# Kernel tuning notes

Measured on AMD Instinct MI355X. Metric: run time of the kernel, lower is better.

## Reference

```python
import jax, jax.numpy as jnp
import numpy as np

NEG_INF = float(np.finfo(np.float32).min)
CHUNK = 8
EPS = 1e-6
NOISE_STD = 1.0
SHARP = 1.0


def exclusive_cumsum(x):
    # [a,b,c] -> [0,a,a+b]
    return jnp.cumsum(jnp.pad(x[:, :-1], ((0, 0), (1, 0))), axis=1)


def moving_sum(x, back, forward):
    # x: [B, K]; out[i] = sum x[i-back : i+forward+1], via cumsum difference
    w = back + forward + 1
    xp = jnp.pad(x, ((0, 0), (back, forward)))
    cs = jnp.pad(jnp.cumsum(xp, axis=1), ((0, 0), (1, 0)))
    return cs[:, w:] - cs[:, :-w]


def setup_inputs() -> dict:
    key = jax.random.key(0)
    ks = jax.random.split(key, 12)
    B, K, D, A = 64, 2000, 512, 512
    s = 0.02
    inp = {
        'key': jax.random.normal(ks[0], (B, K, D), jnp.float32),
        'value': jax.random.normal(ks[1], (B, K, D), jnp.float32),
        'query': jax.random.normal(ks[2], (B, 1, D), jnp.float32),
        'mask': jnp.ones((B, 1, K), jnp.int32),
        'aw_prev': jnp.zeros((B, K), jnp.float32).at[:, 0].set(1.0),
        'noise': jax.random.normal(ks[3], (B, K), jnp.float32),
        'Wk_mono': jax.random.normal(ks[4], (D, A), jnp.float32) * s,
        'bk_mono': jnp.zeros((A,), jnp.float32),
        'Wq_mono': jax.random.normal(ks[5], (D, A), jnp.float32) * s,
        'bq_mono': jnp.zeros((A,), jnp.float32),
        'r': jnp.full((1,), -4.0, jnp.float32),
        'Wk_chunk': jax.random.normal(ks[6], (D, A), jnp.float32) * s,
        'bk_chunk': jnp.zeros((A,), jnp.float32),
        'Wq_chunk': jax.random.normal(ks[7], (D, A), jnp.float32) * s,
        'bq_chunk': jnp.zeros((A,), jnp.float32),
    }
    return inp


def reference(key, value, query, mask, aw_prev, noise,
              Wk_mono, bk_mono, Wq_mono, bq_mono, r,
              Wk_chunk, bk_chunk, Wq_chunk, bq_chunk):
    B, K, _ = key.shape
    adim = Wk_mono.shape[1]
    scale = jnp.sqrt(jnp.asarray(adim, jnp.float32))
    m = mask.reshape(B, K) != 0  # qlen == 1

    # ---- monotonic energy (scaled_dot) ----
    k_m = key @ Wk_mono + bk_mono              # [B,K,A]
    q_m = query @ Wq_mono + bq_mono            # [B,1,A]
    e_mono = jnp.einsum('bqa,bka->bk', q_m, k_m) / scale + r[0]
    e_mono = jnp.where(m, e_mono, NEG_INF)

    # ---- parallel-mode monotonic alignment ----
    p = jax.nn.sigmoid(e_mono + noise * NOISE_STD)             # p_choose_i
    cumprod_1mp = jnp.exp(exclusive_cumsum(jnp.log(jnp.clip(1.0 - p, EPS, 1.0))))
    alpha = p * cumprod_1mp * jnp.cumsum(
        aw_prev / jnp.clip(cumprod_1mp, EPS, 1.0), axis=1)     # [B,K]

    # ---- chunkwise attention ----
    k_c = key @ Wk_chunk + bk_chunk
    q_c = query @ Wq_chunk + bq_chunk
    e_c = jnp.einsum('bqa,bka->bk', q_c, k_c) / scale
    e_c = jnp.where(m, e_c, NEG_INF)
    e_c = e_c - jnp.max(e_c, axis=1, keepdims=True)
    sm_exp = jnp.clip(jnp.exp(e_c), 1e-5, None)
    denom = moving_sum(sm_exp, CHUNK - 1, 0)
    beta = sm_exp * moving_sum(alpha * SHARP / denom, 0, CHUNK - 1)  # [B,K]

    # ---- context vector ----
    cv = jnp.einsum('bk,bkd->bd', beta, value)[:, None, :]     # [B,1,D]
    return cv, alpha
```

## Files before the change

### kernel.cpp

```cpp
#include <hip/hip_runtime.h>
#include <hip/hip_bf16.h>

#define B_N    64
#define K_LEN  2000
#define D_DIM  512
#define NEG_INF (-3.402823466e38f)
#define EPS_C  1e-6f
#define INV_SCALE (1.0f/22.62741699796952f)

__global__ __launch_bounds__(256) void proj_kernel(
    const float* __restrict__ query,
    const float* __restrict__ Wq_m, const float* __restrict__ bq_m,
    const float* __restrict__ Wq_c, const float* __restrict__ bq_c,
    const float* __restrict__ Wk_m, const float* __restrict__ bk_m,
    const float* __restrict__ Wk_c, const float* __restrict__ bk_c,
    const float* __restrict__ r,
    float* __restrict__ v_all, float* __restrict__ c_all)
{
    const int b = blockIdx.x, br = blockIdx.y, t = threadIdx.x;
    const float* Wq = br ? Wq_c : Wq_m;
    const float* bq = br ? bq_c : bq_m;
    const float* Wk = br ? Wk_c : Wk_m;
    const float* bk = br ? bk_c : bk_m;
    __shared__ float qs[D_DIM];
    __shared__ float qv[D_DIM];
    __shared__ float red[256];
    for (int i = t; i < D_DIM; i += 256) qs[i] = query[(size_t)b*D_DIM + i];
    __syncthreads();
    for (int a = t; a < D_DIM; a += 256) {
        float a0 = 0.f, a1 = 0.f, a2 = 0.f, a3 = 0.f;
        #pragma unroll 4
        for (int d = 0; d < D_DIM; d += 4) {
            a0 = fmaf(qs[d+0], Wq[(size_t)(d+0)*D_DIM + a], a0);
            a1 = fmaf(qs[d+1], Wq[(size_t)(d+1)*D_DIM + a], a1);
            a2 = fmaf(qs[d+2], Wq[(size_t)(d+2)*D_DIM + a], a2);
            a3 = fmaf(qs[d+3], Wq[(size_t)(d+3)*D_DIM + a], a3);
        }
        qv[a] = (a0 + a1) + (a2 + a3) + bq[a];
    }
    __syncthreads();
    for (int d = t; d < D_DIM; d += 256) {
        const float4* row = (const float4*)(Wk + (size_t)d*D_DIM);
        const float4* q4 = (const float4*)qv;
        float acc = 0.f;
        #pragma unroll 4
        for (int a4 = 0; a4 < D_DIM/4; ++a4) {
            float4 w = row[a4], q = q4[a4];
            acc = fmaf(w.x, q.x, acc); acc = fmaf(w.y, q.y, acc);
            acc = fmaf(w.z, q.z, acc); acc = fmaf(w.w, q.w, acc);
        }
        v_all[((size_t)b*2 + br)*D_DIM + d] = acc * INV_SCALE;
    }
    float part = 0.f;
    for (int a = t; a < D_DIM; a += 256) part = fmaf(qv[a], bk[a], part);
    red[t] = part; __syncthreads();
    for (int s = 128; s; s >>= 1) { if (t < s) red[t] += red[t + s]; __syncthreads(); }
    if (t == 0) c_all[b*2 + br] = red[0] * INV_SCALE + (br ? 0.f : r[0]);
}

__global__ __launch_bounds__(256) void energy_kernel(
    const float* __restrict__ key, const int* __restrict__ mask,
    const float* __restrict__ v_all, const float* __restrict__ c_all,
    float* __restrict__ e_mono, float* __restrict__ e_c)
{
    const int b = blockIdx.x;
    const int kb0 = blockIdx.y * 125;
    const int kend = kb0 + 125;
    const int lane = threadIdx.x & 63;
    const int wave = threadIdx.x >> 6;
    const float4* vm4 = (const float4*)(v_all + ((size_t)b*2 + 0)*D_DIM);
    const float4* vc4 = (const float4*)(v_all + ((size_t)b*2 + 1)*D_DIM);
    const float4 vmA = vm4[lane*2], vmB = vm4[lane*2 + 1];
    const float4 vcA = vc4[lane*2], vcB = vc4[lane*2 + 1];
    const float cm = c_all[b*2 + 0], cc = c_all[b*2 + 1];

    for (int k = kb0 + wave; k < kend; k += 8) {
        const int k2 = k + 4;
        const bool has2 = (k2 < kend);
        const float4* kr0 = (const float4*)(key + ((size_t)b*K_LEN + k)*D_DIM);
        const float4* kr1 = (const float4*)(key + ((size_t)b*K_LEN + (has2 ? k2 : k))*D_DIM);
        float4 a0 = kr0[lane*2], b0 = kr0[lane*2 + 1];
        float4 a1 = kr1[lane*2], b1 = kr1[lane*2 + 1];
        float dm0 = 0.f, dc0 = 0.f, dm1 = 0.f, dc1 = 0.f;
        dm0 = fmaf(a0.x, vmA.x, dm0); dm0 = fmaf(a0.y, vmA.y, dm0);
        dm0 = fmaf(a0.z, vmA.z, dm0); dm0 = fmaf(a0.w, vmA.w, dm0);
        dm0 = fmaf(b0.x, vmB.x, dm0); dm0 = fmaf(b0.y, vmB.y, dm0);
        dm0 = fmaf(b0.z, vmB.z, dm0); dm0 = fmaf(b0.w, vmB.w, dm0);
        dc0 = fmaf(a0.x, vcA.x, dc0); dc0 = fmaf(a0.y, vcA.y, dc0);
        dc0 = fmaf(a0.z, vcA.z, dc0); dc0 = fmaf(a0.w, vcA.w, dc0);
        dc0 = fmaf(b0.x, vcB.x, dc0); dc0 = fmaf(b0.y, vcB.y, dc0);
        dc0 = fmaf(b0.z, vcB.z, dc0); dc0 = fmaf(b0.w, vcB.w, dc0);
        dm1 = fmaf(a1.x, vmA.x, dm1); dm1 = fmaf(a1.y, vmA.y, dm1);
        dm1 = fmaf(a1.z, vmA.z, dm1); dm1 = fmaf(a1.w, vmA.w, dm1);
        dm1 = fmaf(b1.x, vmB.x, dm1); dm1 = fmaf(b1.y, vmB.y, dm1);
        dm1 = fmaf(b1.z, vmB.z, dm1); dm1 = fmaf(b1.w, vmB.w, dm1);
        dc1 = fmaf(a1.x, vcA.x, dc1); dc1 = fmaf(a1.y, vcA.y, dc1);
        dc1 = fmaf(a1.z, vcA.z, dc1); dc1 = fmaf(a1.w, vcA.w, dc1);
        dc1 = fmaf(b1.x, vcB.x, dc1); dc1 = fmaf(b1.y, vcB.y, dc1);
        dc1 = fmaf(b1.z, vcB.z, dc1); dc1 = fmaf(b1.w, vcB.w, dc1);
        #pragma unroll
        for (int off = 32; off; off >>= 1) {
            dm0 += __shfl_xor(dm0, off); dc0 += __shfl_xor(dc0, off);
            dm1 += __shfl_xor(dm1, off); dc1 += __shfl_xor(dc1, off);
        }
        if (lane == 0) {
            size_t gk = (size_t)b*K_LEN + k;
            bool mk = mask[gk] != 0;
            e_mono[gk] = mk ? dm0 + cm : NEG_INF;
            e_c[gk]    = mk ? dc0 + cc : NEG_INF;
            if (has2) {
                size_t gk2 = (size_t)b*K_LEN + k2;
                bool mk2 = mask[gk2] != 0;
                e_mono[gk2] = mk2 ? dm1 + cm : NEG_INF;
                e_c[gk2]    = mk2 ? dc1 + cc : NEG_INF;
            }
        }
    }
}

__global__ __launch_bounds__(256) void scan_kernel(
    const float* __restrict__ e_mono_g, const float* __restrict__ e_c_g,
    const float* __restrict__ noise, const float* __restrict__ aw_prev,
    float* __restrict__ alpha_out, float* __restrict__ beta_out)
{
    const int b = blockIdx.x, t = threadIdx.x;
    const int lane = t & 63, wv = t >> 6;
    __shared__ float sal[2048];
    __shared__ float sse[2048];
    __shared__ float su[2048];
    __shared__ float wsA[4], wsB[4], wsM[4];

    const float* em = e_mono_g + (size_t)b*K_LEN;
    const float* ec = e_c_g   + (size_t)b*K_LEN;
    const float* nz = noise   + (size_t)b*K_LEN;
    const float* aw = aw_prev + (size_t)b*K_LEN;

    const int base = t*8;
    float p[8], lg[8];
    #pragma unroll
    for (int j = 0; j < 8; ++j) {
        const int k = base + j;
        float pv = 0.f, lv = 0.f, ecv = NEG_INF;
        if (k < K_LEN) {
            float e = em[k] + nz[k];
            pv = 1.f / (1.f + __expf(-e) * 1.0f);
            pv = 1.f / (1.f + expf(-e));
            float om = fminf(fmaxf(1.f - pv, EPS_C), 1.f);
            lv = logf(om);
            ecv = ec[k];
        }
        p[j] = pv; lg[j] = lv; sse[k] = ecv;
    }

    float ex[8]; float run = 0.f;
    #pragma unroll
    for (int j = 0; j < 8; ++j) { ex[j] = run; run += lg[j]; }
    float incl = run;
    #pragma unroll
    for (int off = 1; off < 64; off <<= 1) {
        float v = __shfl_up(incl, off, 64);
        if (lane >= off) incl += v;
    }
    if (lane == 63) wsA[wv] = incl;
    __syncthreads();
    float wpre = 0.f;
    #pragma unroll
    for (int w = 0; w < 4; ++w) if (w < wv) wpre += wsA[w];
    const float pre = wpre + incl - run;

    float cp[8], t2i[8]; float run2 = 0.f;
    #pragma unroll
    for (int j = 0; j < 8; ++j) {
        const int k = base + j;
        float c = expf(pre + ex[j]);
        cp[j] = c;
        float t2 = 0.f;
        if (k < K_LEN) t2 = aw[k] / fminf(fmaxf(c, EPS_C), 1.f);
        run2 += t2; t2i[j] = run2;
    }
    float incl2 = run2;
    #pragma unroll
    for (int off = 1; off < 64; off <<= 1) {
        float v = __shfl_up(incl2, off, 64);
        if (lane >= off) incl2 += v;
    }
    if (lane == 63) wsB[wv] = incl2;
    __syncthreads();
    float wpre2 = 0.f;
    #pragma unroll
    for (int w = 0; w < 4; ++w) if (w < wv) wpre2 += wsB[w];
    const float pre2 = wpre2 + incl2 - run2;
    #pragma unroll
    for (int j = 0; j < 8; ++j) {
        const int k = base + j;
        float al = p[j] * cp[j] * (pre2 + t2i[j]);
        sal[k] = al;
        if (k < K_LEN) alpha_out[(size_t)b*K_LEN + k] = al;
    }
    __syncthreads();

    float mx = NEG_INF;
    for (int k = t; k < 2048; k += 256) mx = fmaxf(mx, sse[k]);
    #pragma unroll
    for (int off = 32; off; off >>= 1) mx = fmaxf(mx, __shfl_xor(mx, off));
    if (lane == 0) wsM[wv] = mx;
    __syncthreads();
    mx = fmaxf(fmaxf(wsM[0], wsM[1]), fmaxf(wsM[2], wsM[3]));

    for (int k = t; k < 2048; k += 256) {
        float se = 0.f;
        if (k < K_LEN) se = fmaxf(expf(sse[k] - mx), 1e-5f);
        sse[k] = se;
    }
    __syncthreads();
    for (int k = t; k < 2048; k += 256) {
        float u = 0.f;
        if (k < K_LEN) {
            float den = 0.f;
            int j0 = (k > 7) ? (k - 7) : 0;
            for (int j = j0; j <= k; ++j) den += sse[j];
            u = sal[k] / den;
        }
        su[k] = u;
    }
    __syncthreads();
    for (int k = t; k < K_LEN; k += 256) {
        float s2 = 0.f;
        #pragma unroll
        for (int j = 0; j < 8; ++j) s2 += su[k + j];
        beta_out[(size_t)b*K_LEN + k] = sse[k] * s2;
    }
}

__global__ __launch_bounds__(256) void cv_part_kernel(
    const float* __restrict__ value, const float* __restrict__ beta,
    float* __restrict__ partial)
{
    const int b = blockIdx.x, s = blockIdx.y, t = threadIdx.x;
    const int f4 = t & 127, half = t >> 7;
    const int k0 = s * 100;
    __shared__ float bs[100];
    __shared__ float4 comb[128];
    if (t < 100) bs[t] = beta[(size_t)b*K_LEN + k0 + t];
    __syncthreads();
    float4 acc = {0.f, 0.f, 0.f, 0.f};
    for (int k = k0 + half; k < k0 + 100; k += 2) {
        float4 vv = ((const float4*)(value + ((size_t)b*K_LEN + k)*D_DIM))[f4];
        float bb = bs[k - k0];
        acc.x = fmaf(bb, vv.x, acc.x); acc.y = fmaf(bb, vv.y, acc.y);
        acc.z = fmaf(bb, vv.z, acc.z); acc.w = fmaf(bb, vv.w, acc.w);
    }
    if (half) comb[f4] = acc;
    __syncthreads();
    if (!half) {
        float4 o = comb[f4];
        acc.x += o.x; acc.y += o.y; acc.z += o.z; acc.w += o.w;
        ((float4*)(partial + ((size_t)b*20 + s)*D_DIM))[f4] = acc;
    }
}

__global__ __launch_bounds__(256) void cv_reduce_kernel(
    const float* __restrict__ partial, float* __restrict__ cv)
{
    const int idx = blockIdx.x*256 + threadIdx.x;
    const int b = idx >> 9, d = idx & 511;
    float acc = 0.f;
    #pragma unroll
    for (int s = 0; s < 20; ++s) acc += partial[((size_t)b*20 + s)*D_DIM + d];
    cv[idx] = acc;
}

extern "C" void kernel_launch(void* const* d_in, const int* in_sizes, int n_in,
                              void* d_out, int out_size, void* d_ws, size_t ws_size,
                              hipStream_t stream) {
    const float* key     = (const float*)d_in[0];
    const float* value   = (const float*)d_in[1];
    const float* query   = (const float*)d_in[2];
    const int*   mask    = (const int*)d_in[3];
    const float* aw_prev = (const float*)d_in[4];
    const float* noise   = (const float*)d_in[5];
    const float* Wk_m    = (const float*)d_in[6];
    const float* bk_m    = (const float*)d_in[7];
    const float* Wq_m    = (const float*)d_in[8];
    const float* bq_m    = (const float*)d_in[9];
    const float* r       = (const float*)d_in[10];
    const float* Wk_c    = (const float*)d_in[11];
    const float* bk_c    = (const float*)d_in[12];
    const float* Wq_c    = (const float*)d_in[13];
    const float* bq_c    = (const float*)d_in[14];

    float* out   = (float*)d_out;
    float* cv    = out;
    float* alpha = out + (size_t)B_N*D_DIM;

    float* ws      = (float*)d_ws;
    float* e_mono  = ws;
    float* e_c     = ws + 128000;
    float* beta    = ws + 256000;
    float* v_all   = ws + 384000;
    float* c_all   = ws + 449536;
    float* partial = ws + 449664;

    proj_kernel<<<dim3(B_N, 2), 256, 0, stream>>>(query, Wq_m, bq_m, Wq_c, bq_c,
                                                  Wk_m, bk_m, Wk_c, bk_c, r,
                                                  v_all, c_all);
    energy_kernel<<<dim3(B_N, 16), 256, 0, stream>>>(key, mask, v_all, c_all, e_mono, e_c);
    scan_kernel<<<B_N, 256, 0, stream>>>(e_mono, e_c, noise, aw_prev, alpha, beta);
    cv_part_kernel<<<dim3(B_N, 20), 256, 0, stream>>>(value, beta, partial);
    cv_reduce_kernel<<<32768/256, 256, 0, stream>>>(partial, cv);
}
```

Baseline: 613.2 us.

## Coalesce key loads, widen scan block, unroll cv loop, replace reduce with atomics

The energy kernel now reads key rows in fully contiguous float4 strides (lane and 64+lane) instead of interleaved pairs, with the query vectors permuted to match. The scan kernel moves to 512 threads, each handling 4 elements, to shorten per-thread serial work. The context-vector kernel unrolls two rows per iteration and accumulates straight into the output with atomicAdd after a memset, which removes the separate reduce kernel and its partial buffer. Atomics make the float summation order nondeterministic and add one memset launch.

New measurement: 621.7 us. About the same (+1.4%).

```diff
diff --git a/kernel.cpp b/kernel.cpp
--- a/kernel.cpp
+++ b/kernel.cpp
@@ -70,8 +70,8 @@
     const int wave = threadIdx.x >> 6;
     const float4* vm4 = (const float4*)(v_all + ((size_t)b*2 + 0)*D_DIM);
     const float4* vc4 = (const float4*)(v_all + ((size_t)b*2 + 1)*D_DIM);
-    const float4 vmA = vm4[lane*2], vmB = vm4[lane*2 + 1];
-    const float4 vcA = vc4[lane*2], vcB = vc4[lane*2 + 1];
+    const float4 vmA = vm4[lane], vmB = vm4[64 + lane];
+    const float4 vcA = vc4[lane], vcB = vc4[64 + lane];
     const float cm = c_all[b*2 + 0], cc = c_all[b*2 + 1];
 
     for (int k = kb0 + wave; k < kend; k += 8) {
@@ -79,8 +79,8 @@
         const bool has2 = (k2 < kend);
         const float4* kr0 = (const float4*)(key + ((size_t)b*K_LEN + k)*D_DIM);
         const float4* kr1 = (const float4*)(key + ((size_t)b*K_LEN + (has2 ? k2 : k))*D_DIM);
-        float4 a0 = kr0[lane*2], b0 = kr0[lane*2 + 1];
-        float4 a1 = kr1[lane*2], b1 = kr1[lane*2 + 1];
+        float4 a0 = kr0[lane], b0 = kr0[64 + lane];
+        float4 a1 = kr1[lane], b1 = kr1[64 + lane];
         float dm0 = 0.f, dc0 = 0.f, dm1 = 0.f, dc1 = 0.f;
         dm0 = fmaf(a0.x, vmA.x, dm0); dm0 = fmaf(a0.y, vmA.y, dm0);
         dm0 = fmaf(a0.z, vmA.z, dm0); dm0 = fmaf(a0.w, vmA.w, dm0);
@@ -118,7 +118,7 @@
     }
 }
 
-__global__ __launch_bounds__(256) void scan_kernel(
+__global__ __launch_bounds__(512) void scan_kernel(
     const float* __restrict__ e_mono_g, const float* __restrict__ e_c_g,
     const float* __restrict__ noise, const float* __restrict__ aw_prev,
     float* __restrict__ alpha_out, float* __restrict__ beta_out)
@@ -128,22 +128,21 @@
     __shared__ float sal[2048];
     __shared__ float sse[2048];
     __shared__ float su[2048];
-    __shared__ float wsA[4], wsB[4], wsM[4];
+    __shared__ float wsA[8], wsB[8], wsM[8];
 
     const float* em = e_mono_g + (size_t)b*K_LEN;
     const float* ec = e_c_g   + (size_t)b*K_LEN;
     const float* nz = noise   + (size_t)b*K_LEN;
     const float* aw = aw_prev + (size_t)b*K_LEN;
 
-    const int base = t*8;
-    float p[8], lg[8];
-    #pragma unroll
-    for (int j = 0; j < 8; ++j) {
+    const int base = t*4;
+    float p[4], lg[4];
+    #pragma unroll
+    for (int j = 0; j < 4; ++j) {
         const int k = base + j;
         float pv = 0.f, lv = 0.f, ecv = NEG_INF;
         if (k < K_LEN) {
             float e = em[k] + nz[k];
-            pv = 1.f / (1.f + __expf(-e) * 1.0f);
             pv = 1.f / (1.f + expf(-e));
             float om = fminf(fmaxf(1.f - pv, EPS_C), 1.f);
             lv = logf(om);
@@ -152,9 +151,9 @@
         p[j] = pv; lg[j] = lv; sse[k] = ecv;
     }
 
-    float ex[8]; float run = 0.f;
-    #pragma unroll
-    for (int j = 0; j < 8; ++j) { ex[j] = run; run += lg[j]; }
+    float ex[4]; float run = 0.f;
+    #pragma unroll
+    for (int j = 0; j < 4; ++j) { ex[j] = run; run += lg[j]; }
     float incl = run;
     #pragma unroll
     for (int off = 1; off < 64; off <<= 1) {
@@ -165,12 +164,12 @@
     __syncthreads();
     float wpre = 0.f;
     #pragma unroll
-    for (int w = 0; w < 4; ++w) if (w < wv) wpre += wsA[w];
+    for (int w = 0; w < 8; ++w) if (w < wv) wpre += wsA[w];
     const float pre = wpre + incl - run;
 
-    float cp[8], t2i[8]; float run2 = 0.f;
-    #pragma unroll
-    for (int j = 0; j < 8; ++j) {
+    float cp[4], t2i[4]; float run2 = 0.f;
+    #pragma unroll
+    for (int j = 0; j < 4; ++j) {
         const int k = base + j;
         float c = expf(pre + ex[j]);
         cp[j] = c;
@@ -188,10 +187,10 @@
     __syncthreads();
     float wpre2 = 0.f;
     #pragma unroll
-    for (int w = 0; w < 4; ++w) if (w < wv) wpre2 += wsB[w];
+    for (int w = 0; w < 8; ++w) if (w < wv) wpre2 += wsB[w];
     const float pre2 = wpre2 + incl2 - run2;
     #pragma unroll
-    for (int j = 0; j < 8; ++j) {
+    for (int j = 0; j < 4; ++j) {
         const int k = base + j;
         float al = p[j] * cp[j] * (pre2 + t2i[j]);
         sal[k] = al;
@@ -200,20 +199,22 @@
     __syncthreads();
 
     float mx = NEG_INF;
-    for (int k = t; k < 2048; k += 256) mx = fmaxf(mx, sse[k]);
+    for (int k = t; k < 2048; k += 512) mx = fmaxf(mx, sse[k]);
     #pragma unroll
     for (int off = 32; off; off >>= 1) mx = fmaxf(mx, __shfl_xor(mx, off));
     if (lane == 0) wsM[wv] = mx;
     __syncthreads();
-    mx = fmaxf(fmaxf(wsM[0], wsM[1]), fmaxf(wsM[2], wsM[3]));
-
-    for (int k = t; k < 2048; k += 256) {
+    mx = wsM[0];
+    #pragma unroll
+    for (int w = 1; w < 8; ++w) mx = fmaxf(mx, wsM[w]);
+
+    for (int k = t; k < 2048; k += 512) {
         float se = 0.f;
         if (k < K_LEN) se = fmaxf(expf(sse[k] - mx), 1e-5f);
         sse[k] = se;
     }
     __syncthreads();
-    for (int k = t; k < 2048; k += 256) {
+    for (int k = t; k < 2048; k += 512) {
         float u = 0.f;
         if (k < K_LEN) {
             float den = 0.f;
@@ -224,7 +225,7 @@
         su[k] = u;
     }
     __syncthreads();
-    for (int k = t; k < K_LEN; k += 256) {
+    for (int k = t; k < K_LEN; k += 512) {
         float s2 = 0.f;
         #pragma unroll
         for (int j = 0; j < 8; ++j) s2 += su[k + j];
@@ -234,40 +235,36 @@
 
 __global__ __launch_bounds__(256) void cv_part_kernel(
     const float* __restrict__ value, const float* __restrict__ beta,
-    float* __restrict__ partial)
+    float* __restrict__ cv)
 {
     const int b = blockIdx.x, s = blockIdx.y, t = threadIdx.x;
-    const int f4 = t & 127, half = t >> 7;
+    const int f4 = t & 127, rp = t >> 7;
     const int k0 = s * 100;
     __shared__ float bs[100];
     __shared__ float4 comb[128];
     if (t < 100) bs[t] = beta[(size_t)b*K_LEN + k0 + t];
     __syncthreads();
-    float4 acc = {0.f, 0.f, 0.f, 0.f};
-    for (int k = k0 + half; k < k0 + 100; k += 2) {
-        float4 vv = ((const float4*)(value + ((size_t)b*K_LEN + k)*D_DIM))[f4];
-        float bb = bs[k - k0];
-        acc.x = fmaf(bb, vv.x, acc.x); acc.y = fmaf(bb, vv.y, acc.y);
-        acc.z = fmaf(bb, vv.z, acc.z); acc.w = fmaf(bb, vv.w, acc.w);
-    }
-    if (half) comb[f4] = acc;
-    __syncthreads();
-    if (!half) {
+    float4 acc0 = {0.f, 0.f, 0.f, 0.f}, acc1 = {0.f, 0.f, 0.f, 0.f};
+    for (int k = k0 + rp; k < k0 + 100; k += 4) {
+        float4 v0 = ((const float4*)(value + ((size_t)b*K_LEN + k)*D_DIM))[f4];
+        float4 v1 = ((const float4*)(value + ((size_t)b*K_LEN + k + 2)*D_DIM))[f4];
+        float b0 = bs[k - k0], b1 = bs[k - k0 + 2];
+        acc0.x = fmaf(b0, v0.x, acc0.x); acc0.y = fmaf(b0, v0.y, acc0.y);
+        acc0.z = fmaf(b0, v0.z, acc0.z); acc0.w = fmaf(b0, v0.w, acc0.w);
+        acc1.x = fmaf(b1, v1.x, acc1.x); acc1.y = fmaf(b1, v1.y, acc1.y);
+        acc1.z = fmaf(b1, v1.z, acc1.z); acc1.w = fmaf(b1, v1.w, acc1.w);
+    }
+    acc0.x += acc1.x; acc0.y += acc1.y; acc0.z += acc1.z; acc0.w += acc1.w;
+    if (rp) comb[f4] = acc0;
+    __syncthreads();
+    if (!rp) {
         float4 o = comb[f4];
-        acc.x += o.x; acc.y += o.y; acc.z += o.z; acc.w += o.w;
-        ((float4*)(partial + ((size_t)b*20 + s)*D_DIM))[f4] = acc;
-    }
-}
-
-__global__ __launch_bounds__(256) void cv_reduce_kernel(
-    const float* __restrict__ partial, float* __restrict__ cv)
-{
-    const int idx = blockIdx.x*256 + threadIdx.x;
-    const int b = idx >> 9, d = idx & 511;
-    float acc = 0.f;
-    #pragma unroll
-    for (int s = 0; s < 20; ++s) acc += partial[((size_t)b*20 + s)*D_DIM + d];
-    cv[idx] = acc;
+        float* dst = cv + (size_t)b*D_DIM + f4*4;
+        atomicAdd(dst + 0, acc0.x + o.x);
+        atomicAdd(dst + 1, acc0.y + o.y);
+        atomicAdd(dst + 2, acc0.z + o.z);
+        atomicAdd(dst + 3, acc0.w + o.w);
+    }
 }
 
 extern "C" void kernel_launch(void* const* d_in, const int* in_sizes, int n_in,
@@ -299,13 +296,13 @@
     float* beta    = ws + 256000;
     float* v_all   = ws + 384000;
     float* c_all   = ws + 449536;
-    float* partial = ws + 449664;
+
+    hipMemsetAsync(cv, 0, (size_t)B_N*D_DIM*sizeof(float), stream);
 
     proj_kernel<<<dim3(B_N, 2), 256, 0, stream>>>(query, Wq_m, bq_m, Wq_c, bq_c,
                                                   Wk_m, bk_m, Wk_c, bk_c, r,
                                                   v_all, c_all);
     energy_kernel<<<dim3(B_N, 16), 256, 0, stream>>>(key, mask, v_all, c_all, e_mono, e_c);
-    scan_kernel<<<B_N, 256, 0, stream>>>(e_mono, e_c, noise, aw_prev, alpha, beta);
-    cv_part_kernel<<<dim3(B_N, 20), 256, 0, stream>>>(value, beta, partial);
-    cv_reduce_kernel<<<32768/256, 256, 0, stream>>>(partial, cv);
-}
+    scan_kernel<<<B_N, 512, 0, stream>>>(e_mono, e_c, noise, aw_prev, alpha, beta);
+    cv_part_kernel<<<dim3(B_N, 20), 256, 0, stream>>>(value, beta, cv);
+}
```
